# Performance work log

Hardware: AMD Instinct MI355X
Metric: run time of the kernel (lower is better)

## Reference

```python
import jax, jax.numpy as jnp
import numpy as np

L = 16            # table_num (levels)
LOG2T = 14
T = 1 << LOG2T    # entries per table
Z = 512           # z_dim
S = 256           # style_dim
IMG = 256         # img_size
RES_MIN, RES_MAX = 16, 256
HID, OUT = 64, 3  # mlp hidden / out dims
B = 8
FDIM = 2 * L      # retrieved feature dim (2 per level)
PRIME = jnp.uint32(2654435761)  # instant-ngp hash prime
GAIN = 1.4142135623730951       # stylegan lrelu gain sqrt(2)
# geometric level resolutions res_min -> res_max
RES = np.floor(RES_MIN * np.exp(np.arange(L) * np.log(RES_MAX / RES_MIN) / (L - 1))).astype(np.float32)


def _lrelu(x):
    return GAIN * jnp.where(x >= 0, x, 0.2 * x)


def _coords():
    c = (jnp.arange(IMG, dtype=jnp.float32) + 0.5) / IMG
    x, y = jnp.meshgrid(c, c, indexing='ij')
    return jnp.stack((x, y), -1).reshape(-1, 2)  # (N, 2), N = IMG*IMG


def _mod_linear(x, s, aw, ab, w, b):
    # StyleGAN2-style modulated linear with demodulation. x: (B,N,in), s: (B,S)
    style = s @ aw + ab                                   # (B, in)
    demod = jax.lax.rsqrt((style ** 2) @ (w ** 2) + 1e-8)  # (B, out)
    return ((x * style[:, None, :]) @ w) * demod[:, None, :] + b


def _forward(z, mw0, mb0, mw1, mb1, mw2, mb2, base_tables, w_mod, b_mod,
             a0w, a0b, w0, bb0, a1w, a1b, w1, bb1, a2w, a2b, w2, bb2):
    s = _lrelu(z @ mw0 + mb0)
    s = _lrelu(s @ mw1 + mb1)
    s = _lrelu(s @ mw2 + mb2)                              # (B, S)
    # style-conditioned hash tables: per-level per-channel modulation of base tables
    scale = 1.0 + (s @ w_mod + b_mod).reshape(-1, L, 1, 2)
    tables = base_tables[None] * scale                     # (B, L, T, 2)

    coords = _coords()                                     # (N, 2)
    offs = jnp.array([[0, 0], [1, 0], [0, 1], [1, 1]], dtype=jnp.uint32)
    feats = []
    for l in range(L):
        pos = coords * RES[l]
        p0 = jnp.floor(pos)
        frac = pos - p0                                    # (N, 2)
        p0i = p0.astype(jnp.uint32)
        cx = p0i[None, :, 0] + offs[:, 0:1]                # (4, N)
        cy = p0i[None, :, 1] + offs[:, 1:2]
        idx = ((cx ^ (cy * PRIME)) & jnp.uint32(T - 1)).astype(jnp.int32)  # (4, N)
        wx = jnp.where(offs[:, 0:1] == 1, frac[None, :, 0], 1.0 - frac[None, :, 0])
        wy = jnp.where(offs[:, 1:2] == 1, frac[None, :, 1], 1.0 - frac[None, :, 1])
        wgt = wx * wy                                      # (4, N)
        tl = tables[:, l]                                  # (B, T, 2)
        f = jnp.take(tl, idx.reshape(-1), axis=1).reshape(tl.shape[0], 4, -1, 2)
        feats.append(jnp.einsum('bcnd,cn->bnd', f, wgt))   # bilinear interp
    h = jnp.concatenate(feats, -1)                         # (B, N, 2L)

    # stacked modulated MLP (3 layers), final tanh, then render to image
    h = _lrelu(_mod_linear(h, s, a0w, a0b, w0, bb0))
    h = _lrelu(_mod_linear(h, s, a1w, a1b, w1, bb1))
    h = jnp.tanh(_mod_linear(h, s, a2w, a2b, w2, bb2))     # (B, N, 3)
    return h.reshape(-1, IMG, IMG, OUT).transpose(0, 3, 1, 2)


def setup_inputs() -> dict:
    key = jax.random.key(0)
    ks = jax.random.split(key, 12)
    nrm = lambda k, sh, sc: jax.random.normal(k, sh, jnp.float32) * sc
    inp = {}
    inp['z'] = jax.random.normal(ks[0], (B, Z), jnp.float32)
    inp['mw0'] = nrm(ks[1], (Z, S), 1 / np.sqrt(Z)); inp['mb0'] = jnp.zeros((S,), jnp.float32)
    inp['mw1'] = nrm(ks[2], (S, S), 1 / np.sqrt(S)); inp['mb1'] = jnp.zeros((S,), jnp.float32)
    inp['mw2'] = nrm(ks[3], (S, S), 1 / np.sqrt(S)); inp['mb2'] = jnp.zeros((S,), jnp.float32)
    inp['base_tables'] = nrm(ks[4], (L, T, 2), 0.1)
    inp['w_mod'] = nrm(ks[5], (S, L * 2), 1 / np.sqrt(S)); inp['b_mod'] = jnp.zeros((L * 2,), jnp.float32)
    inp['a0w'] = nrm(ks[6], (S, FDIM), 1 / np.sqrt(S)); inp['a0b'] = jnp.ones((FDIM,), jnp.float32)
    inp['w0'] = nrm(ks[7], (FDIM, HID), 1 / np.sqrt(FDIM)); inp['bb0'] = jnp.zeros((HID,), jnp.float32)
    inp['a1w'] = nrm(ks[8], (S, HID), 1 / np.sqrt(S)); inp['a1b'] = jnp.ones((HID,), jnp.float32)
    inp['w1'] = nrm(ks[9], (HID, HID), 1 / np.sqrt(HID)); inp['bb1'] = jnp.zeros((HID,), jnp.float32)
    inp['a2w'] = nrm(ks[10], (S, HID), 1 / np.sqrt(S)); inp['a2b'] = jnp.ones((HID,), jnp.float32)
    inp['w2'] = nrm(ks[11], (HID, OUT), 1 / np.sqrt(HID)); inp['bb2'] = jnp.zeros((OUT,), jnp.float32)
    return inp


def reference(z, mw0, mb0, mw1, mb1, mw2, mb2, base_tables, w_mod, b_mod,
              a0w, a0b, w0, bb0, a1w, a1b, w1, bb1, a2w, a2b, w2, bb2):
    return _forward(z, mw0, mb0, mw1, mb1, mw2, mb2, base_tables, w_mod, b_mod,
                    a0w, a0b, w0, bb0, a1w, a1b, w1, bb1, a2w, a2b, w2, bb2)
```

## Files before the change

### kernel.cpp

```cpp
#include <hip/hip_runtime.h>
#include <hip/hip_bf16.h>

#define NLVL 16
#define TSZ  16384
#define NB   8

typedef _Float16 h8 __attribute__((ext_vector_type(8)));
typedef float    f4 __attribute__((ext_vector_type(4)));

#define MFMA16(A,B,C) __builtin_amdgcn_mfma_f32_16x16x32_f16(A,B,C,0,0,0)
#define GAINF 1.41421356237309515f

__device__ constexpr float RES_TAB[16] = {
  16.f, 19.f, 23.f, 27.f, 33.f, 40.f, 48.f, 58.f,
  70.f, 84.f, 101.f, 122.f, 147.f, 176.f, 212.f, 255.f
};

__device__ __forceinline__ float lrelu(float x) {
  float v = x < 0.0f ? 0.2f * x : x;
  return GAINF * v;
}
__device__ __forceinline__ float act(float x) { return fmaxf(x, 0.2f * x); }

__device__ __forceinline__ float tanh_fast(float x) {
  float t = __builtin_amdgcn_exp2f(x * 2.8853900817779268f);
  return 1.0f - 2.0f * __builtin_amdgcn_rcpf(t + 1.0f);
}

__device__ __forceinline__ unsigned pk(float a, float b) {
  union { decltype(__builtin_amdgcn_cvt_pkrtz(0.f, 0.f)) h; unsigned u; } U;
  U.h = __builtin_amdgcn_cvt_pkrtz(a, b);
  return U.u;
}

__device__ __forceinline__ void hash_features(const float* __restrict__ bt,
                                              int n, float* g)
{
  const float inv = 1.0f / 256.0f;
  float cx = ((n >> 8) + 0.5f) * inv;
  float cy = ((n & 255) + 0.5f) * inv;
#pragma unroll
  for (int l = 0; l < NLVL; ++l) {
    float res = RES_TAB[l];
    float px = cx * res, py = cy * res;
    float fx0 = floorf(px), fy0 = floorf(py);
    float fx = px - fx0, fy = py - fy0;
    unsigned x0 = (unsigned)fx0, y0 = (unsigned)fy0;
    unsigned hy0 = y0 * 2654435761u;
    unsigned hy1 = (y0 + 1u) * 2654435761u;
    unsigned i00 = (x0 ^ hy0) & 16383u;
    unsigned i10 = ((x0 + 1u) ^ hy0) & 16383u;
    unsigned i01 = (x0 ^ hy1) & 16383u;
    unsigned i11 = ((x0 + 1u) ^ hy1) & 16383u;
    const float2* tb = (const float2*)(bt + (size_t)l * (TSZ * 2));
    float2 f00 = tb[i00], f10 = tb[i10], f01 = tb[i01], f11 = tb[i11];
    float wx0 = 1.0f - fx, wy0 = 1.0f - fy;
    float w00 = wx0 * wy0, w10 = fx * wy0, w01 = wx0 * fy, w11 = fx * fy;
    g[2 * l]     = w00 * f00.x + w10 * f10.x + w01 * f01.x + w11 * f11.x;
    g[2 * l + 1] = w00 * f00.y + w10 * f10.y + w01 * f01.y + w11 * f11.y;
  }
}

__device__ __forceinline__ void pf_slice(const float* __restrict__ p, int nf4,
                                         int s, int t, uint2& sink)
{
  int per = nf4 >> 5;
  const uint4* q = (const uint4*)p + (size_t)s * per;
  for (int e = t; e < per; e += 256) {
    uint4 v = q[e];
    sink.x ^= v.x; sink.y ^= v.w;
  }
}

__device__ __forceinline__ void map_layer(const float* __restrict__ xs_in,
                                          float* __restrict__ out_lds,
                                          const float* __restrict__ W,
                                          const float* __restrict__ bias,
                                          int K, int t,
                                          float* __restrict__ part)
{
  const int j4 = (t & 63) * 4;
  const int ks = t >> 6;
  const int chunk = K >> 2;
  const int kb = ks * chunk;
  f4 a0 = {0,0,0,0}, a1 = {0,0,0,0}, a2 = {0,0,0,0}, a3 = {0,0,0,0};
#pragma unroll 4
  for (int k = 0; k < chunk; k += 4) {
    f4 w0 = *(const f4*)&W[(kb + k + 0) * 256 + j4];
    f4 w1 = *(const f4*)&W[(kb + k + 1) * 256 + j4];
    f4 w2 = *(const f4*)&W[(kb + k + 2) * 256 + j4];
    f4 w3 = *(const f4*)&W[(kb + k + 3) * 256 + j4];
    float x0 = xs_in[kb + k + 0], x1 = xs_in[kb + k + 1];
    float x2 = xs_in[kb + k + 2], x3 = xs_in[kb + k + 3];
    a0 += x0 * w0; a1 += x1 * w1; a2 += x2 * w2; a3 += x3 * w3;
  }
  *(f4*)&part[ks * 256 + j4] = (a0 + a1) + (a2 + a3);
  __syncthreads();
  {
    float v = part[t] + part[256 + t] + part[512 + t] + part[768 + t];
    out_lds[t] = lrelu(bias[t] + v);
  }
  __syncthreads();
}

__global__ void __launch_bounds__(256) k_pre(
    const float* __restrict__ z,
    const float* __restrict__ mw0, const float* __restrict__ mb0,
    const float* __restrict__ mw1, const float* __restrict__ mb1,
    const float* __restrict__ mw2, const float* __restrict__ mb2,
    const float* __restrict__ bt,
    const float* __restrict__ w_mod, const float* __restrict__ b_mod,
    const float* __restrict__ a0w, const float* __restrict__ a0b,
    const float* __restrict__ w0,
    const float* __restrict__ a1w, const float* __restrict__ a1b,
    const float* __restrict__ w1,
    const float* __restrict__ a2w, const float* __restrict__ a2b,
    const float* __restrict__ w2,
    _Float16* __restrict__ W0h, _Float16* __restrict__ W1h,
    _Float16* __restrict__ W2h, _Float16* __restrict__ ghf)
{
  __shared__ float xs[512];
  __shared__ float sA[256], sB[256];
  __shared__ float part[1024];
  __shared__ float st0[32], scf[32], st1[64], st2[64];
  __shared__ float dm0[64], dm1[64], dm2[3];

  const int t = threadIdx.x;

  if (blockIdx.x >= 8) {
    int s = (blockIdx.x - 8) >> 3;
    uint2 sink = {0, 0};
    pf_slice(mw0,  32768, s, t, sink);
    pf_slice(mw1,  16384, s, t, sink);
    pf_slice(mw2,  16384, s, t, sink);
    pf_slice(w_mod, 2048, s, t, sink);
    pf_slice(a0w,   2048, s, t, sink);
    pf_slice(a1w,   4096, s, t, sink);
    pf_slice(a2w,   4096, s, t, sink);
    pf_slice(w0,     512, s, t, sink);
    pf_slice(w1,    1024, s, t, sink);
    if (s == 0) {
      const uint4* q = (const uint4*)w2;
      for (int e = t; e < 48; e += 256) { uint4 v = q[e]; sink.x ^= v.x; }
      const uint4* qb = (const uint4*)mb0;
      for (int e = t; e < 64; e += 256) { uint4 v = qb[e]; sink.y ^= v.y; }
    }
    asm volatile("" :: "v"(sink.x), "v"(sink.y));

    int n = (blockIdx.x - 8) * 256 + t;
    float gl[32];
    hash_features(bt, n, gl);
    int tile = n >> 4, c = n & 15;
#pragma unroll
    for (int gg = 0; gg < 4; ++gg) {
      union { unsigned u[4]; uint4 v; } U;
      U.u[0] = pk(gl[8 * gg + 0], gl[8 * gg + 1]);
      U.u[1] = pk(gl[8 * gg + 2], gl[8 * gg + 3]);
      U.u[2] = pk(gl[8 * gg + 4], gl[8 * gg + 5]);
      U.u[3] = pk(gl[8 * gg + 6], gl[8 * gg + 7]);
      *(uint4*)&ghf[(size_t)tile * 512 + (gg * 16 + c) * 8] = U.v;
    }
    return;
  }

  const int b = blockIdx.x;

  for (int k = t; k < 512; k += 256) xs[k] = z[b * 512 + k];
  __syncthreads();

  map_layer(xs, sA, mw0, mb0, 512, t, part);
  map_layer(sA, sB, mw1, mb1, 256, t, part);
  map_layer(sB, xs, mw2, mb2, 256, t, part);
  const float* ss = xs;

  {
    const int j = t & 31, kb = (t >> 5) * 32;
    float am = 0.f, as = 0.f;
#pragma unroll 8
    for (int k = 0; k < 32; ++k) {
      float sv = ss[kb + k];
      am = fmaf(sv, w_mod[(kb + k) * 32 + j], am);
      as = fmaf(sv, a0w[(kb + k) * 32 + j], as);
    }
    part[t] = am; part[256 + t] = as;
  }
  {
    const int j = t & 63, kb = (t >> 6) * 64;
    float v1 = 0.f, v2 = 0.f;
#pragma unroll 8
    for (int k = 0; k < 64; ++k) {
      float sv = ss[kb + k];
      v1 = fmaf(sv, a1w[(kb + k) * 64 + j], v1);
      v2 = fmaf(sv, a2w[(kb + k) * 64 + j], v2);
    }
    part[512 + t] = v1; part[768 + t] = v2;
  }
  __syncthreads();
  if (t < 32) {
    float am = b_mod[t], as = a0b[t];
#pragma unroll
    for (int q = 0; q < 8; ++q) { am += part[q * 32 + t]; as += part[256 + q * 32 + t]; }
    scf[t] = 1.0f + am; st0[t] = as;
  }
  if (t >= 128 && t < 192) {
    int j = t - 128;
    float v1 = a1b[j], v2 = a2b[j];
#pragma unroll
    for (int q = 0; q < 4; ++q) { v1 += part[512 + q * 64 + j]; v2 += part[768 + q * 64 + j]; }
    st1[j] = v1; st2[j] = v2;
  }
  __syncthreads();

  if (t < 64) {
    float acc = 1e-8f;
    for (int i = 0; i < 32; ++i) { float p = st0[i] * w0[i * 64 + t]; acc = fmaf(p, p, acc); }
    dm0[t] = 1.0f / sqrtf(acc);
  }
  if (t >= 64 && t < 128) {
    int j = t - 64; float acc = 1e-8f;
    for (int k = 0; k < 64; ++k) { float p = st1[k] * w1[k * 64 + j]; acc = fmaf(p, p, acc); }
    dm1[j] = 1.0f / sqrtf(acc);
  }
  if (t >= 192 && t < 195) {
    int ch = t - 192; float acc = 1e-8f;
    for (int k = 0; k < 64; ++k) { float p = st2[k] * w2[k * 3 + ch]; acc = fmaf(p, p, acc); }
    dm2[ch] = 1.0f / sqrtf(acc);
  }
  __syncthreads();

  for (int f = t; f < 2048; f += 256) {
    int j = f >> 5, i = f & 31;
    W0h[b * 2048 + f] = (_Float16)(scf[i] * st0[i] * w0[i * 64 + j] * dm0[j]);
  }
  for (int f = t; f < 4096; f += 256) {
    int j2 = f >> 6, k = f & 63;
    W1h[b * 4096 + f] = (_Float16)(GAINF * st1[k] * w1[k * 64 + j2] * dm1[j2]);
  }
  for (int f = t; f < 1024; f += 256) {
    int ch = f >> 6, k = f & 63;
    W2h[b * 1024 + f] = (ch < 3) ? (_Float16)(GAINF * st2[k] * w2[k * 3 + ch] * dm2[ch])
                                 : (_Float16)0.0f;
  }
}

__device__ __forceinline__ void st4(_Float16* L, int pix, int jb, f4 v) {
  int ks = jb ^ ((pix & 7) << 3);
  union { unsigned u[2]; uint2 v2; } U;
  U.u[0] = pk(v[0], v[1]); U.u[1] = pk(v[2], v[3]);
  *(uint2*)(L + pix * 64 + ks) = U.v2;
}
__device__ __forceinline__ h8 ldf(const _Float16* L, int pix, int kb) {
  int ks = kb ^ ((pix & 7) << 3);
  return *(const h8*)(L + pix * 64 + ks);
}

template <int FUSED>
__global__ void __launch_bounds__(256) k_mlp(
    const _Float16* __restrict__ W0h, const _Float16* __restrict__ W1h,
    const _Float16* __restrict__ W2h, const _Float16* __restrict__ ghf,
    const float* __restrict__ bt,
    const float* __restrict__ bb0, const float* __restrict__ bb1,
    const float* __restrict__ bb2, float* __restrict__ out)
{
  __shared__ _Float16 lds[4][4096];
  __shared__ _Float16 hb[FUSED ? 8192 : 8];

  const int t = threadIdx.x;
  const int w = t >> 6, lane = t & 63;
  const int c = lane & 15, g = lane >> 4;
  const int b = blockIdx.y;
  const int pixb = blockIdx.x * 256 + w * 64;
  const int tile0 = pixb >> 4;
  _Float16* L = lds[w];

  if constexpr (FUSED) {
    float gl[32];
    hash_features(bt, blockIdx.x * 256 + t, gl);
    int tl = t >> 4, cl = t & 15;
#pragma unroll
    for (int gg = 0; gg < 4; ++gg) {
      union { unsigned u[4]; uint4 v; } U;
      U.u[0] = pk(gl[8 * gg + 0], gl[8 * gg + 1]);
      U.u[1] = pk(gl[8 * gg + 2], gl[8 * gg + 3]);
      U.u[2] = pk(gl[8 * gg + 4], gl[8 * gg + 5]);
      U.u[3] = pk(gl[8 * gg + 6], gl[8 * gg + 7]);
      *(uint4*)&hb[tl * 512 + (gg * 16 + cl) * 8] = U.v;
    }
    __syncthreads();
  }

  h8 A0[4], A1[4][2], A2[2];
#pragma unroll
  for (int jt = 0; jt < 4; ++jt)
    A0[jt] = *(const h8*)&W0h[b * 2048 + (jt * 16 + c) * 32 + 8 * g];
#pragma unroll
  for (int jt = 0; jt < 4; ++jt)
#pragma unroll
    for (int kf = 0; kf < 2; ++kf)
      A1[jt][kf] = *(const h8*)&W1h[b * 4096 + (jt * 16 + c) * 64 + kf * 32 + 8 * g];
#pragma unroll
  for (int kf = 0; kf < 2; ++kf)
    A2[kf] = *(const h8*)&W2h[b * 1024 + c * 64 + kf * 32 + 8 * g];

  f4 bv0[4], bv1[4], bv2;
#pragma unroll
  for (int jt = 0; jt < 4; ++jt) {
    bv0[jt] = *(const f4*)&bb0[jt * 16 + 4 * g];
    bv1[jt] = *(const f4*)&bb1[jt * 16 + 4 * g];
  }
  if (g == 0) { bv2 = f4{bb2[0], bb2[1], bb2[2], 0.0f}; }
  else        { bv2 = f4{0.0f, 0.0f, 0.0f, 0.0f}; }

  f4 acc[4][4];
#pragma unroll
  for (int pt = 0; pt < 4; ++pt) {
    h8 Bh;
    if constexpr (FUSED) {
      Bh = *(const h8*)&hb[(w * 4 + pt) * 512 + lane * 8];
    } else {
      Bh = *(const h8*)&ghf[(size_t)(tile0 + pt) * 512 + lane * 8];
    }
#pragma unroll
    for (int jt = 0; jt < 4; ++jt)
      acc[jt][pt] = MFMA16(A0[jt], Bh, bv0[jt]);
  }

#pragma unroll
  for (int jt = 0; jt < 4; ++jt)
#pragma unroll
    for (int pt = 0; pt < 4; ++pt) {
      f4 v = acc[jt][pt];
#pragma unroll
      for (int r = 0; r < 4; ++r) v[r] = act(v[r]);
      st4(L, pt * 16 + c, jt * 16 + 4 * g, v);
    }

  f4 acc1[4][4];
#pragma unroll
  for (int pt = 0; pt < 4; ++pt) {
    h8 Bf0 = ldf(L, pt * 16 + c, 0 * 32 + 8 * g);
    h8 Bf1 = ldf(L, pt * 16 + c, 1 * 32 + 8 * g);
#pragma unroll
    for (int jt = 0; jt < 4; ++jt) {
      f4 a = MFMA16(A1[jt][0], Bf0, bv1[jt]);
      acc1[jt][pt] = MFMA16(A1[jt][1], Bf1, a);
    }
  }

#pragma unroll
  for (int jt = 0; jt < 4; ++jt)
#pragma unroll
    for (int pt = 0; pt < 4; ++pt) {
      f4 v = acc1[jt][pt];
#pragma unroll
      for (int r = 0; r < 4; ++r) v[r] = act(v[r]);
      st4(L, pt * 16 + c, jt * 16 + 4 * g, v);
    }

#pragma unroll
  for (int pt = 0; pt < 4; ++pt) {
    h8 Bf0 = ldf(L, pt * 16 + c, 0 * 32 + 8 * g);
    h8 Bf1 = ldf(L, pt * 16 + c, 1 * 32 + 8 * g);
    f4 a = MFMA16(A2[0], Bf0, bv2);
    a = MFMA16(A2[1], Bf1, a);
    if (g == 0) {
      int pix = pixb + pt * 16 + c;
#pragma unroll
      for (int r = 0; r < 3; ++r)
        out[((b * 3 + r) << 16) + pix] = tanh_fast(a[r]);
    }
  }
}

extern "C" void kernel_launch(void* const* d_in, const int* in_sizes, int n_in,
                              void* d_out, int out_size, void* d_ws, size_t ws_size,
                              hipStream_t stream)
{
  const float* z    = (const float*)d_in[0];
  const float* mw0  = (const float*)d_in[1];
  const float* mb0  = (const float*)d_in[2];
  const float* mw1  = (const float*)d_in[3];
  const float* mb1  = (const float*)d_in[4];
  const float* mw2  = (const float*)d_in[5];
  const float* mb2  = (const float*)d_in[6];
  const float* bt   = (const float*)d_in[7];
  const float* wmod = (const float*)d_in[8];
  const float* bmod = (const float*)d_in[9];
  const float* a0w  = (const float*)d_in[10];
  const float* a0b  = (const float*)d_in[11];
  const float* w0   = (const float*)d_in[12];
  const float* bb0  = (const float*)d_in[13];
  const float* a1w  = (const float*)d_in[14];
  const float* a1b  = (const float*)d_in[15];
  const float* w1   = (const float*)d_in[16];
  const float* bb1  = (const float*)d_in[17];
  const float* a2w  = (const float*)d_in[18];
  const float* a2b  = (const float*)d_in[19];
  const float* w2   = (const float*)d_in[20];
  const float* bb2  = (const float*)d_in[21];

  char* ws = (char*)d_ws;
  _Float16* W0h = (_Float16*)(ws);
  _Float16* W1h = (_Float16*)(ws + 32768);
  _Float16* W2h = (_Float16*)(ws + 98304);
  _Float16* ghf = (_Float16*)(ws + 114688);
  float* out = (float*)d_out;

  k_pre<<<8 + 256, 256, 0, stream>>>(z, mw0, mb0, mw1, mb1, mw2, mb2, bt,
                                     wmod, bmod, a0w, a0b, w0,
                                     a1w, a1b, w1, a2w, a2b, w2,
                                     W0h, W1h, W2h, ghf);

  if (ws_size >= (size_t)4308992) {
    k_mlp<0><<<dim3(256, NB), 256, 0, stream>>>(W0h, W1h, W2h, ghf, bt,
                                                bb0, bb1, bb2, out);
  } else {
    k_mlp<1><<<dim3(256, NB), 256, 0, stream>>>(W0h, W1h, W2h, ghf, bt,
                                                bb0, bb1, bb2, out);
  }
}
```

Measured before the change: 45.32 us.

## Split hash-feature blocks per level group and drop weight-prefetch warming

The hash-feature precompute blocks now each handle one group of four levels for 256 pixels, so 1024 blocks run instead of 256 blocks doing all sixteen levels. This gives more parallelism and fewer live registers per thread. The L2-warming reads of the mapping and MLP weights are removed. The fallback path now launches only the style blocks, since that path computes hash features inside the MLP kernel. Dropping the prefetch may expose cold weight loads in the 8 style blocks, which sit on the critical path.

```diff
diff --git a/kernel.cpp b/kernel.cpp
--- a/kernel.cpp
+++ b/kernel.cpp
@@ -11,7 +11,7 @@
 #define MFMA16(A,B,C) __builtin_amdgcn_mfma_f32_16x16x32_f16(A,B,C,0,0,0)
 #define GAINF 1.41421356237309515f
 
-__device__ constexpr float RES_TAB[16] = {
+__device__ const float RES_TAB[16] = {
   16.f, 19.f, 23.f, 27.f, 33.f, 40.f, 48.f, 58.f,
   70.f, 84.f, 101.f, 122.f, 147.f, 176.f, 212.f, 255.f
 };
@@ -33,15 +33,15 @@
   return U.u;
 }
 
-__device__ __forceinline__ void hash_features(const float* __restrict__ bt,
-                                              int n, float* g)
+__device__ __forceinline__ void hash4(const float* __restrict__ bt,
+                                      int n, int l0, float* g8)
 {
   const float inv = 1.0f / 256.0f;
   float cx = ((n >> 8) + 0.5f) * inv;
   float cy = ((n & 255) + 0.5f) * inv;
 #pragma unroll
-  for (int l = 0; l < NLVL; ++l) {
-    float res = RES_TAB[l];
+  for (int j = 0; j < 4; ++j) {
+    float res = RES_TAB[l0 + j];
     float px = cx * res, py = cy * res;
     float fx0 = floorf(px), fy0 = floorf(py);
     float fx = px - fx0, fy = py - fy0;
@@ -52,24 +52,20 @@
     unsigned i10 = ((x0 + 1u) ^ hy0) & 16383u;
     unsigned i01 = (x0 ^ hy1) & 16383u;
     unsigned i11 = ((x0 + 1u) ^ hy1) & 16383u;
-    const float2* tb = (const float2*)(bt + (size_t)l * (TSZ * 2));
+    const float2* tb = (const float2*)(bt + (size_t)(l0 + j) * (TSZ * 2));
     float2 f00 = tb[i00], f10 = tb[i10], f01 = tb[i01], f11 = tb[i11];
     float wx0 = 1.0f - fx, wy0 = 1.0f - fy;
     float w00 = wx0 * wy0, w10 = fx * wy0, w01 = wx0 * fy, w11 = fx * fy;
-    g[2 * l]     = w00 * f00.x + w10 * f10.x + w01 * f01.x + w11 * f11.x;
-    g[2 * l + 1] = w00 * f00.y + w10 * f10.y + w01 * f01.y + w11 * f11.y;
-  }
-}
-
-__device__ __forceinline__ void pf_slice(const float* __restrict__ p, int nf4,
-                                         int s, int t, uint2& sink)
-{
-  int per = nf4 >> 5;
-  const uint4* q = (const uint4*)p + (size_t)s * per;
-  for (int e = t; e < per; e += 256) {
-    uint4 v = q[e];
-    sink.x ^= v.x; sink.y ^= v.w;
-  }
+    g8[2 * j]     = w00 * f00.x + w10 * f10.x + w01 * f01.x + w11 * f11.x;
+    g8[2 * j + 1] = w00 * f00.y + w10 * f10.y + w01 * f01.y + w11 * f11.y;
+  }
+}
+
+__device__ __forceinline__ void hash_features(const float* __restrict__ bt,
+                                              int n, float* g)
+{
+#pragma unroll
+  for (int q = 0; q < 4; ++q) hash4(bt, n, q * 4, g + 8 * q);
 }
 
 __device__ __forceinline__ void map_layer(const float* __restrict__ xs_in,
@@ -128,38 +124,18 @@
   const int t = threadIdx.x;
 
   if (blockIdx.x >= 8) {
-    int s = (blockIdx.x - 8) >> 3;
-    uint2 sink = {0, 0};
-    pf_slice(mw0,  32768, s, t, sink);
-    pf_slice(mw1,  16384, s, t, sink);
-    pf_slice(mw2,  16384, s, t, sink);
-    pf_slice(w_mod, 2048, s, t, sink);
-    pf_slice(a0w,   2048, s, t, sink);
-    pf_slice(a1w,   4096, s, t, sink);
-    pf_slice(a2w,   4096, s, t, sink);
-    pf_slice(w0,     512, s, t, sink);
-    pf_slice(w1,    1024, s, t, sink);
-    if (s == 0) {
-      const uint4* q = (const uint4*)w2;
-      for (int e = t; e < 48; e += 256) { uint4 v = q[e]; sink.x ^= v.x; }
-      const uint4* qb = (const uint4*)mb0;
-      for (int e = t; e < 64; e += 256) { uint4 v = qb[e]; sink.y ^= v.y; }
-    }
-    asm volatile("" :: "v"(sink.x), "v"(sink.y));
-
-    int n = (blockIdx.x - 8) * 256 + t;
-    float gl[32];
-    hash_features(bt, n, gl);
+    int hb = blockIdx.x - 8;
+    int lg = hb & 3;
+    int n  = (hb >> 2) * 256 + t;
+    float g8[8];
+    hash4(bt, n, lg * 4, g8);
     int tile = n >> 4, c = n & 15;
-#pragma unroll
-    for (int gg = 0; gg < 4; ++gg) {
-      union { unsigned u[4]; uint4 v; } U;
-      U.u[0] = pk(gl[8 * gg + 0], gl[8 * gg + 1]);
-      U.u[1] = pk(gl[8 * gg + 2], gl[8 * gg + 3]);
-      U.u[2] = pk(gl[8 * gg + 4], gl[8 * gg + 5]);
-      U.u[3] = pk(gl[8 * gg + 6], gl[8 * gg + 7]);
-      *(uint4*)&ghf[(size_t)tile * 512 + (gg * 16 + c) * 8] = U.v;
-    }
+    union { unsigned u[4]; uint4 v; } U;
+    U.u[0] = pk(g8[0], g8[1]);
+    U.u[1] = pk(g8[2], g8[3]);
+    U.u[2] = pk(g8[4], g8[5]);
+    U.u[3] = pk(g8[6], g8[7]);
+    *(uint4*)&ghf[(size_t)tile * 512 + (lg * 16 + c) * 8] = U.v;
     return;
   }
 
@@ -406,15 +382,18 @@
   _Float16* ghf = (_Float16*)(ws + 114688);
   float* out = (float*)d_out;
 
-  k_pre<<<8 + 256, 256, 0, stream>>>(z, mw0, mb0, mw1, mb1, mw2, mb2, bt,
-                                     wmod, bmod, a0w, a0b, w0,
-                                     a1w, a1b, w1, a2w, a2b, w2,
-                                     W0h, W1h, W2h, ghf);
-
   if (ws_size >= (size_t)4308992) {
+    k_pre<<<8 + 1024, 256, 0, stream>>>(z, mw0, mb0, mw1, mb1, mw2, mb2, bt,
+                                        wmod, bmod, a0w, a0b, w0,
+                                        a1w, a1b, w1, a2w, a2b, w2,
+                                        W0h, W1h, W2h, ghf);
     k_mlp<0><<<dim3(256, NB), 256, 0, stream>>>(W0h, W1h, W2h, ghf, bt,
                                                 bb0, bb1, bb2, out);
   } else {
+    k_pre<<<8, 256, 0, stream>>>(z, mw0, mb0, mw1, mb1, mw2, mb2, bt,
+                                 wmod, bmod, a0w, a0b, w0,
+                                 a1w, a1b, w1, a2w, a2b, w2,
+                                 W0h, W1h, W2h, ghf);
     k_mlp<1><<<dim3(256, NB), 256, 0, stream>>>(W0h, W1h, W2h, ghf, bt,
                                                 bb0, bb1, bb2, out);
   }
```

New measurement: 49.61 us. +9.5%, slower.
